# Kernel optimization log

Measured on AMD Instinct MI355X. Metric: run time of the kernel, lower is better.

The kernel has to match this reference:

```python
import jax, jax.numpy as jnp
import numpy as np

B, L, D = 64, 512, 768

def setup_inputs() -> dict:
    key = jax.random.key(0)
    k1, k2, k3, k4 = jax.random.split(key, 4)
    hidden_states = jax.random.normal(k1, (B, L, D), dtype=jnp.float32)
    # nn.Linear(hidden_size, hidden_size): weight [D, D], bias [D]
    W = jax.random.normal(k2, (D, D), dtype=jnp.float32) * (1.0 / np.sqrt(D))
    b = jax.random.normal(k3, (D,), dtype=jnp.float32) * 0.02
    # context_vector: [D, 1]
    context_vector = jax.random.normal(k4, (D, 1), dtype=jnp.float32)
    return {"hidden_states": hidden_states, "W": W, "b": b, "context_vector": context_vector}

def reference(hidden_states, W, b, context_vector):
    # tanh(dense(h)): [B, L, D]; torch Linear uses x @ W.T + b
    proj = jnp.tanh(jnp.einsum('bld,ed->ble', hidden_states, W) + b)
    # scores: [B, L]
    scores = jnp.einsum('bld,d->bl', proj, context_vector[:, 0])
    # softmax over sequence dim (dim=1)
    attention_weights = jax.nn.softmax(scores, axis=1)
    # weighted sum over sequence: [B, D]
    weighted_output = jnp.einsum('bld,bl->bd', hidden_states, attention_weights)
    return (weighted_output, attention_weights)
```

## Files before the change

kernel.cpp:

```cpp
#include <hip/hip_runtime.h>
#include <hip/hip_bf16.h>


using half8 = __attribute__((ext_vector_type(8))) _Float16;
using f32x4 = __attribute__((ext_vector_type(4))) float;

#define AS1 __attribute__((address_space(1)))
#define AS3 __attribute__((address_space(3)))

__device__ __forceinline__ void gload_lds16(const void* g, void* l) {
  __builtin_amdgcn_global_load_lds((const AS1 void*)g, (AS3 void*)l, 16, 0, 0);
}

__device__ __forceinline__ unsigned short f2h(float x) {
  _Float16 h = (_Float16)x;
  return __builtin_bit_cast(unsigned short, h);
}


__global__ void convert_h(const float4* __restrict__ H4, ushort4* __restrict__ Ah) {
  int i = blockIdx.x * 256 + threadIdx.x;
  float4 x = H4[i];
  ushort4 o;
  o.x = f2h(x.x); o.y = f2h(x.y); o.z = f2h(x.z); o.w = f2h(x.w);
  Ah[i] = o;
}

__global__ void convert_w(const float4* __restrict__ W4, ushort4* __restrict__ Wt) {
  int i = blockIdx.x * 256 + threadIdx.x;
  float4 x = W4[i];
  ushort4 o;
  o.x = f2h(x.x); o.y = f2h(x.y); o.z = f2h(x.z); o.w = f2h(x.w);
  Wt[i] = o;
}

__global__ __launch_bounds__(256) void gemm_scores(
    const ushort* __restrict__ Ah, const ushort* __restrict__ Wt,
    const float* __restrict__ bias, const float* __restrict__ cvec,
    float* __restrict__ part) {
  __shared__ ushort ldsA[128 * 64];
  __shared__ ushort ldsB[128 * 64];
  __shared__ float scpart[2][128];

  const int tid = threadIdx.x;
  const int lane = tid & 63;
  const int wid = tid >> 6;
  const int wr = wid >> 1, wc = wid & 1;
  const int m = lane & 15, q = lane >> 4;

  const int bid = blockIdx.x;
  const int xcd = bid & 7;
  const int slot = bid >> 3;
  const int mtile = xcd * 32 + slot / 6;
  const int ntile = slot % 6;

  f32x4 acc[4][4];
  #pragma unroll
  for (int a = 0; a < 4; ++a)
    #pragma unroll
    for (int b2 = 0; b2 < 4; ++b2)
      acc[a][b2] = (f32x4){0.f, 0.f, 0.f, 0.f};

  const char* const abase0 = (const char*)Ah + (size_t)(mtile * 128) * 1536;
  const char* const bbase0 = (const char*)Wt + (size_t)(ntile * 128) * 1536;
  char* const ldsAw = (char*)ldsA + (wid << 10);
  char* const ldsBw = (char*)ldsB + (wid << 10);

  for (int kb = 0; kb < 12; ++kb) {
    const char* abase = abase0 + kb * 128;
    const char* bbase = bbase0 + kb * 128;

    #pragma unroll
    for (int r = 0; r < 4; ++r) {
      int off = tid * 16 + r * 4096;
      int row = off >> 7;
      int col = (off & 127) ^ ((row & 7) << 4);
      gload_lds16(abase + row * 1536 + col, ldsAw + r * 4096);
    }
    #pragma unroll
    for (int r = 0; r < 4; ++r) {
      int off = tid * 16 + r * 4096;
      int row = off >> 7;
      int col = (off & 127) ^ ((row & 7) << 4);
      gload_lds16(bbase + row * 1536 + col, ldsBw + r * 4096);
    }
    __syncthreads();

    #pragma unroll
    for (int ks = 0; ks < 2; ++ks) {
      half8 areg[4], breg[4];
      #pragma unroll
      for (int mi = 0; mi < 4; ++mi) {
        int row = wr * 64 + mi * 16 + m;
        int col = (ks * 64 + q * 16) ^ ((row & 7) << 4);
        areg[mi] = *(const half8*)((const char*)ldsA + row * 128 + col);
      }
      #pragma unroll
      for (int ni = 0; ni < 4; ++ni) {
        int row = wc * 64 + ni * 16 + m;
        int col = (ks * 64 + q * 16) ^ ((row & 7) << 4);
        breg[ni] = *(const half8*)((const char*)ldsB + row * 128 + col);
      }
      #pragma unroll
      for (int mi = 0; mi < 4; ++mi)
        #pragma unroll
        for (int ni = 0; ni < 4; ++ni)
          acc[mi][ni] = __builtin_amdgcn_mfma_f32_16x16x32_f16(
              areg[mi], breg[ni], acc[mi][ni], 0, 0, 0);
    }
    __syncthreads();
  }

  float bb[4], cc[4];
  #pragma unroll
  for (int ni = 0; ni < 4; ++ni) {
    int e = ntile * 128 + wc * 64 + ni * 16 + m;
    bb[ni] = bias[e];
    cc[ni] = cvec[e];
  }
  #pragma unroll
  for (int mi = 0; mi < 4; ++mi) {
    #pragma unroll
    for (int j = 0; j < 4; ++j) {
      float s = 0.f;
      #pragma unroll
      for (int ni = 0; ni < 4; ++ni)
        s += tanhf(acc[mi][ni][j] + bb[ni]) * cc[ni];
      s += __shfl_xor(s, 1);
      s += __shfl_xor(s, 2);
      s += __shfl_xor(s, 4);
      s += __shfl_xor(s, 8);
      if (m == 0) scpart[wc][wr * 64 + mi * 16 + q * 4 + j] = s;
    }
  }
  __syncthreads();
  if (tid < 128)
    part[ntile * 32768 + mtile * 128 + tid] = scpart[0][tid] + scpart[1][tid];
}

__global__ void softmax_k(const float* __restrict__ part, float* __restrict__ attn) {
  int b = blockIdx.x, l = threadIdx.x;
  int r = b * 512 + l;
  float s = part[r] + part[32768 + r] + part[2 * 32768 + r] +
            part[3 * 32768 + r] + part[4 * 32768 + r] + part[5 * 32768 + r];
  __shared__ float redm[8], reds[8];
  float mx = s;
  #pragma unroll
  for (int o = 32; o >= 1; o >>= 1) mx = fmaxf(mx, __shfl_xor(mx, o));
  if ((l & 63) == 0) redm[l >> 6] = mx;
  __syncthreads();
  mx = redm[0];
  #pragma unroll
  for (int i = 1; i < 8; ++i) mx = fmaxf(mx, redm[i]);
  float e = expf(s - mx);
  float sm = e;
  #pragma unroll
  for (int o = 32; o >= 1; o >>= 1) sm += __shfl_xor(sm, o);
  if ((l & 63) == 0) reds[l >> 6] = sm;
  __syncthreads();
  float tot = reds[0];
  #pragma unroll
  for (int i = 1; i < 8; ++i) tot += reds[i];
  attn[r] = e / tot;
}

__global__ void wsum_k(const _Float16* __restrict__ Ah, const float* __restrict__ attn,
                       float* __restrict__ out) {
  int b = blockIdx.x, dc = blockIdx.y;
  int t = threadIdx.x;
  __shared__ float w[512];
  w[t] = attn[b * 512 + t];
  w[t + 256] = attn[b * 512 + 256 + t];
  __syncthreads();
  int d = dc * 256 + t;
  const _Float16* hp = Ah + (size_t)b * 512 * 768 + d;
  float acc = 0.f;
  #pragma unroll 8
  for (int l = 0; l < 512; ++l) acc += (float)hp[(size_t)l * 768] * w[l];
  out[b * 768 + d] = acc;
}

extern "C" void kernel_launch(void* const* d_in, const int* in_sizes, int n_in,
                              void* d_out, int out_size, void* d_ws, size_t ws_size,
                              hipStream_t stream) {
  const float* H    = (const float*)d_in[0];
  const float* W    = (const float*)d_in[1];
  const float* bias = (const float*)d_in[2];
  const float* cvec = (const float*)d_in[3];
  float* out = (float*)d_out;

  char* ws = (char*)d_ws;
  ushort* Ah = (ushort*)(ws + 0);
  ushort* Wt = (ushort*)(ws + 50331648);
  float*  prt = (float*)(ws + 51511296);

  hipLaunchKernelGGL(convert_h, dim3(24576), dim3(256), 0, stream,
                     (const float4*)H, (ushort4*)Ah);
  hipLaunchKernelGGL(convert_w, dim3(576), dim3(256), 0, stream,
                     (const float4*)W, (ushort4*)Wt);
  hipLaunchKernelGGL(gemm_scores, dim3(1536), dim3(256), 0, stream,
                     Ah, Wt, bias, cvec, prt);
  hipLaunchKernelGGL(softmax_k, dim3(64), dim3(512), 0, stream, prt, out + 49152);
  hipLaunchKernelGGL(wsum_k, dim3(64, 3), dim3(256), 0, stream,
                     (const _Float16*)Ah, out + 49152, out);
}
```

Measured before the change: 124.1 us.

## Double-buffer GEMM LDS tiles, use fast tanh, and vectorize weighted-sum loads

```diff
diff --git a/kernel.cpp b/kernel.cpp
--- a/kernel.cpp
+++ b/kernel.cpp
@@ -15,6 +15,10 @@
 __device__ __forceinline__ unsigned short f2h(float x) {
   _Float16 h = (_Float16)x;
   return __builtin_bit_cast(unsigned short, h);
+}
+
+__device__ __forceinline__ float tanh_fast(float x) {
+  return 1.0f - __fdividef(2.0f, 1.0f + __expf(2.0f * x));
 }
 
 
@@ -34,12 +38,60 @@
   Wt[i] = o;
 }
 
+
+__device__ __forceinline__ void stage_tiles(const char* abase, const char* bbase,
+                                            char* ldsAbuf, char* ldsBbuf, int tid) {
+  char* ldsAw = ldsAbuf + ((tid >> 6) << 10);
+  char* ldsBw = ldsBbuf + ((tid >> 6) << 10);
+  #pragma unroll
+  for (int r = 0; r < 4; ++r) {
+    int off = tid * 16 + r * 4096;
+    int row = off >> 7;
+    int col = (off & 127) ^ ((row & 7) << 4);
+    gload_lds16(abase + row * 1536 + col, ldsAw + r * 4096);
+  }
+  #pragma unroll
+  for (int r = 0; r < 4; ++r) {
+    int off = tid * 16 + r * 4096;
+    int row = off >> 7;
+    int col = (off & 127) ^ ((row & 7) << 4);
+    gload_lds16(bbase + row * 1536 + col, ldsBw + r * 4096);
+  }
+}
+
+__device__ __forceinline__ void compute_tile(const ushort* ldsAbuf, const ushort* ldsBbuf,
+                                             int wr, int wc, int m, int q,
+                                             f32x4 acc[4][4]) {
+  #pragma unroll
+  for (int ks = 0; ks < 2; ++ks) {
+    half8 areg[4], breg[4];
+    #pragma unroll
+    for (int mi = 0; mi < 4; ++mi) {
+      int row = wr * 64 + mi * 16 + m;
+      int col = (ks * 64 + q * 16) ^ ((row & 7) << 4);
+      areg[mi] = *(const half8*)((const char*)ldsAbuf + row * 128 + col);
+    }
+    #pragma unroll
+    for (int ni = 0; ni < 4; ++ni) {
+      int row = wc * 64 + ni * 16 + m;
+      int col = (ks * 64 + q * 16) ^ ((row & 7) << 4);
+      breg[ni] = *(const half8*)((const char*)ldsBbuf + row * 128 + col);
+    }
+    #pragma unroll
+    for (int mi = 0; mi < 4; ++mi)
+      #pragma unroll
+      for (int ni = 0; ni < 4; ++ni)
+        acc[mi][ni] = __builtin_amdgcn_mfma_f32_16x16x32_f16(
+            areg[mi], breg[ni], acc[mi][ni], 0, 0, 0);
+  }
+}
+
 __global__ __launch_bounds__(256) void gemm_scores(
     const ushort* __restrict__ Ah, const ushort* __restrict__ Wt,
     const float* __restrict__ bias, const float* __restrict__ cvec,
     float* __restrict__ part) {
-  __shared__ ushort ldsA[128 * 64];
-  __shared__ ushort ldsB[128 * 64];
+  __shared__ ushort ldsA[2][8192];
+  __shared__ ushort ldsB[2][8192];
   __shared__ float scpart[2][128];
 
   const int tid = threadIdx.x;
@@ -63,51 +115,21 @@
 
   const char* const abase0 = (const char*)Ah + (size_t)(mtile * 128) * 1536;
   const char* const bbase0 = (const char*)Wt + (size_t)(ntile * 128) * 1536;
-  char* const ldsAw = (char*)ldsA + (wid << 10);
-  char* const ldsBw = (char*)ldsB + (wid << 10);
-
-  for (int kb = 0; kb < 12; ++kb) {
-    const char* abase = abase0 + kb * 128;
-    const char* bbase = bbase0 + kb * 128;
-
-    #pragma unroll
-    for (int r = 0; r < 4; ++r) {
-      int off = tid * 16 + r * 4096;
-      int row = off >> 7;
-      int col = (off & 127) ^ ((row & 7) << 4);
-      gload_lds16(abase + row * 1536 + col, ldsAw + r * 4096);
-    }
-    #pragma unroll
-    for (int r = 0; r < 4; ++r) {
-      int off = tid * 16 + r * 4096;
-      int row = off >> 7;
-      int col = (off & 127) ^ ((row & 7) << 4);
-      gload_lds16(bbase + row * 1536 + col, ldsBw + r * 4096);
-    }
+
+  stage_tiles(abase0, bbase0, (char*)ldsA[0], (char*)ldsB[0], tid);
+  __syncthreads();
+
+  #pragma unroll
+  for (int kb2 = 0; kb2 < 6; ++kb2) {
+    stage_tiles(abase0 + (kb2 * 2 + 1) * 128, bbase0 + (kb2 * 2 + 1) * 128,
+                (char*)ldsA[1], (char*)ldsB[1], tid);
+    compute_tile(ldsA[0], ldsB[0], wr, wc, m, q, acc);
     __syncthreads();
 
-    #pragma unroll
-    for (int ks = 0; ks < 2; ++ks) {
-      half8 areg[4], breg[4];
-      #pragma unroll
-      for (int mi = 0; mi < 4; ++mi) {
-        int row = wr * 64 + mi * 16 + m;
-        int col = (ks * 64 + q * 16) ^ ((row & 7) << 4);
-        areg[mi] = *(const half8*)((const char*)ldsA + row * 128 + col);
-      }
-      #pragma unroll
-      for (int ni = 0; ni < 4; ++ni) {
-        int row = wc * 64 + ni * 16 + m;
-        int col = (ks * 64 + q * 16) ^ ((row & 7) << 4);
-        breg[ni] = *(const half8*)((const char*)ldsB + row * 128 + col);
-      }
-      #pragma unroll
-      for (int mi = 0; mi < 4; ++mi)
-        #pragma unroll
-        for (int ni = 0; ni < 4; ++ni)
-          acc[mi][ni] = __builtin_amdgcn_mfma_f32_16x16x32_f16(
-              areg[mi], breg[ni], acc[mi][ni], 0, 0, 0);
-    }
+    if (kb2 < 5)
+      stage_tiles(abase0 + (kb2 * 2 + 2) * 128, bbase0 + (kb2 * 2 + 2) * 128,
+                  (char*)ldsA[0], (char*)ldsB[0], tid);
+    compute_tile(ldsA[1], ldsB[1], wr, wc, m, q, acc);
     __syncthreads();
   }
 
@@ -125,7 +147,7 @@
       float s = 0.f;
       #pragma unroll
       for (int ni = 0; ni < 4; ++ni)
-        s += tanhf(acc[mi][ni][j] + bb[ni]) * cc[ni];
+        s += tanh_fast(acc[mi][ni][j] + bb[ni]) * cc[ni];
       s += __shfl_xor(s, 1);
       s += __shfl_xor(s, 2);
       s += __shfl_xor(s, 4);
@@ -164,20 +186,26 @@
   attn[r] = e / tot;
 }
 
-__global__ void wsum_k(const _Float16* __restrict__ Ah, const float* __restrict__ attn,
+__global__ void wsum_k(const ushort* __restrict__ Ah, const float* __restrict__ attn,
                        float* __restrict__ out) {
   int b = blockIdx.x, dc = blockIdx.y;
   int t = threadIdx.x;
   __shared__ float w[512];
-  w[t] = attn[b * 512 + t];
-  w[t + 256] = attn[b * 512 + 256 + t];
-  __syncthreads();
-  int d = dc * 256 + t;
-  const _Float16* hp = Ah + (size_t)b * 512 * 768 + d;
-  float acc = 0.f;
+  #pragma unroll
+  for (int i = 0; i < 4; ++i) w[t + i * 128] = attn[b * 512 + t + i * 128];
+  __syncthreads();
+  int d0 = dc * 256 + t * 2;
+  const ushort* hp = Ah + (size_t)b * 512 * 768 + d0;
+  float a0 = 0.f, a1 = 0.f;
   #pragma unroll 8
-  for (int l = 0; l < 512; ++l) acc += (float)hp[(size_t)l * 768] * w[l];
-  out[b * 768 + d] = acc;
+  for (int l = 0; l < 512; ++l) {
+    unsigned u = *(const unsigned*)(hp + (size_t)l * 768);
+    float wl = w[l];
+    a0 += wl * (float)__builtin_bit_cast(_Float16, (unsigned short)(u & 0xffff));
+    a1 += wl * (float)__builtin_bit_cast(_Float16, (unsigned short)(u >> 16));
+  }
+  out[b * 768 + d0] = a0;
+  out[b * 768 + d0 + 1] = a1;
 }
 
 extern "C" void kernel_launch(void* const* d_in, const int* in_sizes, int n_in,
@@ -201,6 +229,6 @@
   hipLaunchKernelGGL(gemm_scores, dim3(1536), dim3(256), 0, stream,
                      Ah, Wt, bias, cvec, prt);
   hipLaunchKernelGGL(softmax_k, dim3(64), dim3(512), 0, stream, prt, out + 49152);
-  hipLaunchKernelGGL(wsum_k, dim3(64, 3), dim3(256), 0, stream,
-                     (const _Float16*)Ah, out + 49152, out);
-}
+  hipLaunchKernelGGL(wsum_k, dim3(64, 3), dim3(128), 0, stream,
+                     Ah, out + 49152, out);
+}
```

New measurement: 112.6 us. 1.1x faster.
